# Optimization experiments

Measured on AMD Instinct MI355X. Metric: run time of the kernel, lower is better.

The kernel has to match this reference:

```python
import jax, jax.numpy as jnp
import numpy as np

D_MODEL = 1024
NUM_HEADS = 16
HEAD_DIM = D_MODEL // NUM_HEADS
NEG = -1e9


def setup_inputs() -> dict:
    key = jax.random.key(0)
    kx, kq, kk, kv, ko = jax.random.split(key, 5)
    scale = 1.0 / np.sqrt(D_MODEL)
    x = jax.random.normal(kx, (4, 2048, D_MODEL), dtype=jnp.float32)
    Wq = jax.random.normal(kq, (D_MODEL, D_MODEL), dtype=jnp.float32) * scale
    Wk = jax.random.normal(kk, (D_MODEL, D_MODEL), dtype=jnp.float32) * scale
    Wv = jax.random.normal(kv, (D_MODEL, D_MODEL), dtype=jnp.float32) * scale
    Wo = jax.random.normal(ko, (D_MODEL, D_MODEL), dtype=jnp.float32) * scale
    return {"x": x, "Wq": Wq, "Wk": Wk, "Wv": Wv, "Wo": Wo}


def reference(x, Wq, Wk, Wv, Wo):
    B, S, _ = x.shape
    # torch Linear: y = x @ W.T
    q = (x @ Wq.T).reshape(B, S, NUM_HEADS, HEAD_DIM).transpose(0, 2, 1, 3)
    k = (x @ Wk.T).reshape(B, S, NUM_HEADS, HEAD_DIM).transpose(0, 2, 1, 3)
    v = (x @ Wv.T).reshape(B, S, NUM_HEADS, HEAD_DIM).transpose(0, 2, 1, 3)
    scores = jnp.einsum("bhqd,bhkd->bhqk", q, k) / jnp.sqrt(jnp.float32(HEAD_DIM))
    # additive causal mask: strictly-upper-triangular entries get -1e9 (as in source)
    mask = jnp.triu(jnp.ones((S, S), dtype=scores.dtype), k=1) * NEG
    scores = scores + mask
    attn = jax.nn.softmax(scores, axis=-1)  # dropout p=0.0 -> identity
    out = jnp.einsum("bhqk,bhkd->bhqd", attn, v)
    out = out.transpose(0, 2, 1, 3).reshape(B, S, D_MODEL)
    return out @ Wo.T
```

## Files before the change

### kernel.cpp

```cpp
#include <hip/hip_runtime.h>

typedef __attribute__((ext_vector_type(8))) short short8;
typedef __attribute__((ext_vector_type(4))) short short4v;
typedef __attribute__((ext_vector_type(4))) unsigned short ushort4v;
typedef __attribute__((ext_vector_type(4))) float f32x4;
typedef __attribute__((ext_vector_type(4))) unsigned int u32x4;

static __device__ __forceinline__ unsigned short f2bf(float f){
  unsigned u = __builtin_bit_cast(unsigned, f);
  unsigned r = u + 0x7fffu + ((u >> 16) & 1u);
  return (unsigned short)(r >> 16);
}

static __device__ __forceinline__ float exp2_fast(float x){
  float r; asm("v_exp_f32 %0, %1" : "=v"(r) : "v"(x)); return r;
}

static __device__ __forceinline__ void g2lds16(const unsigned short* g, unsigned short* l){
  __builtin_amdgcn_global_load_lds(
      (const __attribute__((address_space(1))) void*)g,
      (__attribute__((address_space(3))) void*)l, 16, 0, 0);
}

__global__ __launch_bounds__(256) void cast_bf16_kernel(const float* __restrict__ in,
                                                        unsigned short* __restrict__ out, int n8){
  int i = blockIdx.x * 256 + threadIdx.x;
  if (i >= n8) return;
  const float4* p = (const float4*)in + (size_t)i * 2;
  float4 a = p[0], b = p[1];
  short8 o;
  o[0] = (short)f2bf(a.x); o[1] = (short)f2bf(a.y); o[2] = (short)f2bf(a.z); o[3] = (short)f2bf(a.w);
  o[4] = (short)f2bf(b.x); o[5] = (short)f2bf(b.y); o[6] = (short)f2bf(b.z); o[7] = (short)f2bf(b.w);
  *(short8*)(out + (size_t)i * 8) = o;
}

__global__ __launch_bounds__(256) void cast_w4_kernel(const float* __restrict__ w0,
                                                      const float* __restrict__ w1,
                                                      const float* __restrict__ w2,
                                                      const float* __restrict__ w3,
                                                      unsigned short* __restrict__ o0,
                                                      unsigned short* __restrict__ o1,
                                                      unsigned short* __restrict__ o2,
                                                      unsigned short* __restrict__ o3){
  const int z = blockIdx.y;
  const float* in = (z == 0) ? w0 : (z == 1) ? w1 : (z == 2) ? w2 : w3;
  unsigned short* out = (z == 0) ? o0 : (z == 1) ? o1 : (z == 2) ? o2 : o3;
  int i = blockIdx.x * 256 + threadIdx.x;
  const float4* p = (const float4*)in + (size_t)i * 2;
  float4 a = p[0], b = p[1];
  short8 o;
  o[0] = (short)f2bf(a.x); o[1] = (short)f2bf(a.y); o[2] = (short)f2bf(a.z); o[3] = (short)f2bf(a.w);
  o[4] = (short)f2bf(b.x); o[5] = (short)f2bf(b.y); o[6] = (short)f2bf(b.z); o[7] = (short)f2bf(b.w);
  *(short8*)(out + (size_t)i * 8) = o;
}

template<int MODE>
__global__ __launch_bounds__(256) void gemm_nt(
    const unsigned short* __restrict__ A,
    const unsigned short* __restrict__ B0, const unsigned short* __restrict__ B1,
    const unsigned short* __restrict__ B2,
    unsigned short* __restrict__ q0, unsigned short* __restrict__ q1, unsigned short* __restrict__ q2,
    float* __restrict__ fout,
    int M, int N, int K)
{
  __shared__ __attribute__((aligned(16))) unsigned short As[128 * 64];
  __shared__ __attribute__((aligned(16))) unsigned short Bs[128 * 64];
  const int z = blockIdx.y;
  const unsigned short* __restrict__ B = (z == 0) ? B0 : ((z == 1) ? B1 : B2);
  unsigned short* __restrict__ qo = (z == 0) ? q0 : ((z == 1) ? q1 : q2);
  const int ntn = N >> 7;
  const int nwg = gridDim.x, cpx = nwg >> 3;
  const int bid = blockIdx.x;
  const int swz = (bid & 7) * cpx + (bid >> 3);
  const int tm = swz / ntn, tn = swz % ntn;
  const int m0 = tm << 7, n0 = tn << 7;
  const int t = threadIdx.x;
  const int w = t >> 6;
  const int l = t & 63, lo = l & 15, hi = l >> 4;
  const int wr = w >> 1, wc = w & 1;
  f32x4 acc[4][4];
#pragma unroll
  for (int i = 0; i < 4; ++i)
#pragma unroll
    for (int j = 0; j < 4; ++j) acc[i][j] = (f32x4){0.f, 0.f, 0.f, 0.f};

  const int srow = t >> 3;
  const int us = (l & 7) ^ (srow & 7);
  const unsigned short* gA = A + (size_t)(m0 + srow) * K + us * 8;
  const unsigned short* gB = B + (size_t)(n0 + srow) * K + us * 8;

  const int u0 = (((0 * 4 + hi) ^ (lo & 7)) * 8);
  const int u1 = (((1 * 4 + hi) ^ (lo & 7)) * 8);

  for (int kk = 0; kk < K; kk += 64){
#pragma unroll
    for (int i = 0; i < 4; ++i){
      g2lds16(gA + (size_t)(i * 32) * K + kk, &As[i * 2048 + w * 512]);
      g2lds16(gB + (size_t)(i * 32) * K + kk, &Bs[i * 2048 + w * 512]);
    }
    __syncthreads();
#pragma unroll
    for (int kh = 0; kh < 2; ++kh){
      const int uu = kh ? u1 : u0;
      short8 af[4], bf[4];
#pragma unroll
      for (int mf = 0; mf < 4; ++mf)
        af[mf] = *(const short8*)&As[(wr * 64 + mf * 16 + lo) * 64 + uu];
#pragma unroll
      for (int nf = 0; nf < 4; ++nf)
        bf[nf] = *(const short8*)&Bs[(wc * 64 + nf * 16 + lo) * 64 + uu];
      __builtin_amdgcn_s_setprio(1);
#pragma unroll
      for (int mf = 0; mf < 4; ++mf)
#pragma unroll
        for (int nf = 0; nf < 4; ++nf)
          acc[mf][nf] = __builtin_amdgcn_mfma_f32_16x16x32_bf16(af[mf], bf[nf], acc[mf][nf], 0, 0, 0);
      __builtin_amdgcn_s_setprio(0);
    }
    __syncthreads();
  }

#pragma unroll
  for (int mf = 0; mf < 4; ++mf){
#pragma unroll
    for (int nf = 0; nf < 4; ++nf){
      if (MODE == 0 && z == 2){
        int m = m0 + wr * 64 + mf * 16 + hi * 4;
        int n = n0 + wc * 64 + nf * 16 + lo;
        int b = m >> 11, s = m & 2047, h = n >> 6, d = n & 63;
        ushort4v pk4;
        pk4[0] = f2bf(acc[mf][nf][0]);
        pk4[1] = f2bf(acc[mf][nf][1]);
        pk4[2] = f2bf(acc[mf][nf][2]);
        pk4[3] = f2bf(acc[mf][nf][3]);
        *(ushort4v*)&qo[(((size_t)(b * 16 + h)) * 64 + d) * 2048 + s] = pk4;
      } else {
#pragma unroll
        for (int j = 0; j < 4; ++j){
          int m = m0 + wr * 64 + mf * 16 + hi * 4 + j;
          int n = n0 + wc * 64 + nf * 16 + lo;
          float v = acc[mf][nf][j];
          if (MODE == 0){
            int b = m >> 11, s = m & 2047, h = n >> 6, d = n & 63;
            qo[((((size_t)b * 16 + h) * 2048 + s) << 6) + d] = f2bf(v);
          } else {
            fout[(size_t)m * N + n] = v;
          }
        }
      }
    }
  }
}

__global__ __launch_bounds__(256) void attn_kernel(
    const unsigned short* __restrict__ Q, const unsigned short* __restrict__ K,
    const unsigned short* __restrict__ Vt, unsigned short* __restrict__ O)
{
  __shared__ unsigned short Klds[2][64 * 64];
  __shared__ unsigned short Vlds[2][64 * 64];
  const int bid = blockIdx.x;
  const int xcd = bid & 7, rank = bid >> 3;
  const int bh = xcd * 8 + (rank >> 4);
  const int p = rank & 15;
  const int t = threadIdx.x, w = t >> 6, l = t & 63, lo = l & 15, hi = l >> 4;
  const size_t bb = (size_t)bh * 2048 * 64;
  const int bat = bh >> 4, h = bh & 15;
  const int srow0 = w * 8 + (l >> 3);
  const int su0 = l & 7;
  const float cexp = 0.125f * 1.44269504f;

#define STAGE(bufi, kv0) do { \
  _Pragma("unroll") \
  for (int i_ = 0; i_ < 2; ++i_){ \
    int row_ = i_ * 32 + srow0; \
    int us_ = su0 ^ (row_ & 7); \
    g2lds16(&K[bb + (size_t)((kv0) + row_) * 64 + us_ * 8], &Klds[bufi][i_ * 2048 + w * 512]); \
    g2lds16(&Vt[bb + (size_t)row_ * 2048 + (kv0) + us_ * 8], &Vlds[bufi][i_ * 2048 + w * 512]); \
  } \
} while (0)

#pragma unroll 1
  for (int ph = 0; ph < 2; ++ph){
    const int qt = ph ? (31 - p) : p;
    const int qr = qt * 64 + w * 16;
    short8 aq[2];
#pragma unroll
    for (int kg = 0; kg < 2; ++kg)
      aq[kg] = *(const short8*)&Q[bb + (size_t)(qr + lo) * 64 + kg * 32 + hi * 8];
    f32x4 accO[4];
#pragma unroll
    for (int i = 0; i < 4; ++i) accO[i] = (f32x4){0.f, 0.f, 0.f, 0.f};
    float m2 = -3e38f, lsum = 0.f;

    STAGE(0, 0);
    __syncthreads();
    int buf = 0;

#pragma unroll 1
    for (int s = 0; s <= qt; ++s){
      if (s < qt) STAGE(buf ^ 1, (s + 1) * 64);
      const unsigned short* Kl = &Klds[buf][0];
      const unsigned short* Vl = &Vlds[buf][0];
      f32x4 sa[4];
#pragma unroll
      for (int i = 0; i < 4; ++i) sa[i] = (f32x4){0.f, 0.f, 0.f, 0.f};
      __builtin_amdgcn_s_setprio(1);
#pragma unroll
      for (int ni = 0; ni < 4; ++ni)
#pragma unroll
        for (int kg = 0; kg < 2; ++kg){
          int u = (kg * 4 + hi) ^ (lo & 7);
          short8 kf = *(const short8*)&Kl[(ni * 16 + lo) * 64 + u * 8];
          sa[ni] = __builtin_amdgcn_mfma_f32_16x16x32_bf16(kf, aq[kg], sa[ni], 0, 0, 0);
        }
      __builtin_amdgcn_s_setprio(0);
      if (s == qt){
        const int qg = qr + lo;
        const int kv0 = s * 64;
#pragma unroll
        for (int ni = 0; ni < 4; ++ni)
#pragma unroll
          for (int j = 0; j < 4; ++j){
            int kv = kv0 + ni * 16 + hi * 4 + j;
            if (kv > qg) sa[ni][j] = -1e9f;
          }
      }
      float pm = fmaxf(fmaxf(sa[0][0], sa[0][1]), fmaxf(sa[0][2], sa[0][3]));
      pm = fmaxf(pm, fmaxf(fmaxf(sa[1][0], sa[1][1]), fmaxf(sa[1][2], sa[1][3])));
      pm = fmaxf(pm, fmaxf(fmaxf(sa[2][0], sa[2][1]), fmaxf(sa[2][2], sa[2][3])));
      pm = fmaxf(pm, fmaxf(fmaxf(sa[3][0], sa[3][1]), fmaxf(sa[3][2], sa[3][3])));
      float pms = pm * cexp;
      if (!__all(pms <= m2 + 8.0f)){
        float pr = fmaxf(pms, __shfl_xor(pms, 16, 64));
        pr = fmaxf(pr, __shfl_xor(pr, 32, 64));
        float m2n = fmaxf(m2, pr);
        float corr = exp2_fast(m2 - m2n);
        m2 = m2n;
        lsum *= corr;
        float cj[4];
#pragma unroll
        for (int j = 0; j < 4; ++j) cj[j] = __shfl(corr, hi * 4 + j, 64);
#pragma unroll
        for (int dt = 0; dt < 4; ++dt)
#pragma unroll
          for (int j = 0; j < 4; ++j) accO[dt][j] *= cj[j];
      }
      float rs = 0.f;
#pragma unroll
      for (int ni = 0; ni < 4; ++ni)
#pragma unroll
        for (int j = 0; j < 4; ++j){
          float pv = exp2_fast(fmaf(sa[ni][j], cexp, -m2));
          sa[ni][j] = pv;
          rs += pv;
        }
      rs += __shfl_xor(rs, 16, 64);
      rs += __shfl_xor(rs, 32, 64);
      lsum += rs;
      short8 pa[2];
#pragma unroll
      for (int kg = 0; kg < 2; ++kg){
        unsigned r0, r1, r2, r3;
        asm("v_cvt_pk_bf16_f32 %0, %1, %2" : "=v"(r0) : "v"(sa[2*kg][0]),   "v"(sa[2*kg][1]));
        asm("v_cvt_pk_bf16_f32 %0, %1, %2" : "=v"(r1) : "v"(sa[2*kg][2]),   "v"(sa[2*kg][3]));
        asm("v_cvt_pk_bf16_f32 %0, %1, %2" : "=v"(r2) : "v"(sa[2*kg+1][0]), "v"(sa[2*kg+1][1]));
        asm("v_cvt_pk_bf16_f32 %0, %1, %2" : "=v"(r3) : "v"(sa[2*kg+1][2]), "v"(sa[2*kg+1][3]));
        u32x4 pk; pk[0] = r0; pk[1] = r1; pk[2] = r2; pk[3] = r3;
        pa[kg] = __builtin_bit_cast(short8, pk);
      }
      __builtin_amdgcn_s_setprio(1);
#pragma unroll
      for (int dt = 0; dt < 4; ++dt)
#pragma unroll
        for (int kg = 0; kg < 2; ++kg){
          short4v c0, c1;
          {
            int u = ((kg * 2 + 0) * 2 + (hi >> 1)) ^ (lo & 7);
            c0 = *(const short4v*)&Vl[(dt * 16 + lo) * 64 + u * 8 + (hi & 1) * 4];
          }
          {
            int u = ((kg * 2 + 1) * 2 + (hi >> 1)) ^ (lo & 7);
            c1 = *(const short4v*)&Vl[(dt * 16 + lo) * 64 + u * 8 + (hi & 1) * 4];
          }
          short8 vb = (short8){c0[0], c0[1], c0[2], c0[3], c1[0], c1[1], c1[2], c1[3]};
          accO[dt] = __builtin_amdgcn_mfma_f32_16x16x32_bf16(pa[kg], vb, accO[dt], 0, 0, 0);
        }
      __builtin_amdgcn_s_setprio(0);
      __syncthreads();
      buf ^= 1;
    }
    float lr = 1.0f / lsum;
    float lj[4];
#pragma unroll
    for (int j = 0; j < 4; ++j) lj[j] = __shfl(lr, hi * 4 + j, 64);
#pragma unroll
    for (int dt = 0; dt < 4; ++dt)
#pragma unroll
      for (int j = 0; j < 4; ++j){
        int srow = qr + hi * 4 + j;
        O[((size_t)(bat * 2048 + srow) << 10) + h * 64 + dt * 16 + lo] = f2bf(accO[dt][j] * lj[j]);
      }
  }
#undef STAGE
}

extern "C" void kernel_launch(void* const* d_in, const int* in_sizes, int n_in,
                              void* d_out, int out_size, void* d_ws, size_t ws_size,
                              hipStream_t stream){
  (void)in_sizes; (void)n_in; (void)out_size; (void)ws_size;
  const float* x  = (const float*)d_in[0];
  const float* Wq = (const float*)d_in[1];
  const float* Wk = (const float*)d_in[2];
  const float* Wv = (const float*)d_in[3];
  const float* Wo = (const float*)d_in[4];
  char* ws = (char*)d_ws;
  const size_t MB = 1024 * 1024;
  unsigned short* XB  = (unsigned short*)(ws);
  unsigned short* WQB = (unsigned short*)(ws + 16 * MB);
  unsigned short* WKB = (unsigned short*)(ws + 18 * MB);
  unsigned short* WVB = (unsigned short*)(ws + 20 * MB);
  unsigned short* WOB = (unsigned short*)(ws + 22 * MB);
  unsigned short* Qb  = (unsigned short*)(ws + 24 * MB);
  unsigned short* Kb  = (unsigned short*)(ws + 40 * MB);
  unsigned short* Vtb = (unsigned short*)(ws + 56 * MB);
  unsigned short* Ob  = XB;

  cast_bf16_kernel<<<dim3(4096), 256, 0, stream>>>(x, XB, 8388608 / 8);
  cast_w4_kernel<<<dim3(512, 4), 256, 0, stream>>>(Wq, Wk, Wv, Wo, WQB, WKB, WVB, WOB);

  gemm_nt<0><<<dim3(512, 3), 256, 0, stream>>>(XB, WQB, WKB, WVB, Qb, Kb, Vtb, nullptr,
                                               8192, 1024, 1024);
  attn_kernel<<<dim3(1024), 256, 0, stream>>>(Qb, Kb, Vtb, Ob);
  gemm_nt<1><<<dim3(512, 1), 256, 0, stream>>>(Ob, WOB, WOB, WOB, nullptr, nullptr, nullptr,
                                               (float*)d_out, 8192, 1024, 1024);
}
```

Measured before the change: 173.2 us.

## Add 256x128 triple-buffered 8-wave QKV GEMM with interleaved load/MFMA phases

Replaces the QKV projection GEMM with a new kernel that uses 512 threads, a 256x128 output tile and a three-stage LDS ring buffer filled by direct global-to-LDS loads. Each K step is split into four phases that interleave LDS fragment reads, async prefetch of the stage two steps ahead, and MFMA bursts under raised wave priority, in a ping-pong style schedule. The aim is to hide memory latency and raise MFMA utilisation for the largest GEMM. It uses much more LDS per block (about 144 KB), which limits occupancy to one block per CU and adds many barriers.

```diff
diff --git a/kernel.cpp b/kernel.cpp
--- a/kernel.cpp
+++ b/kernel.cpp
@@ -52,6 +52,167 @@
   o[0] = (short)f2bf(a.x); o[1] = (short)f2bf(a.y); o[2] = (short)f2bf(a.z); o[3] = (short)f2bf(a.w);
   o[4] = (short)f2bf(b.x); o[5] = (short)f2bf(b.y); o[6] = (short)f2bf(b.z); o[7] = (short)f2bf(b.w);
   *(short8*)(out + (size_t)i * 8) = o;
+}
+
+__global__ __launch_bounds__(512) void gemm_qkv_8p(
+    const unsigned short* __restrict__ A,
+    const unsigned short* __restrict__ B0, const unsigned short* __restrict__ B1,
+    const unsigned short* __restrict__ B2,
+    unsigned short* __restrict__ q0, unsigned short* __restrict__ q1, unsigned short* __restrict__ q2,
+    int M, int N, int K)
+{
+  __shared__ __attribute__((aligned(16))) unsigned short As[3][256 * 64];
+  __shared__ __attribute__((aligned(16))) unsigned short Bs[3][128 * 64];
+  const int z = blockIdx.y;
+  const unsigned short* __restrict__ B = (z == 0) ? B0 : ((z == 1) ? B1 : B2);
+  unsigned short* __restrict__ qo = (z == 0) ? q0 : ((z == 1) ? q1 : q2);
+  const int ntn = N >> 7;
+  const int nwg = gridDim.x, cpx = nwg >> 3;
+  const int bid = blockIdx.x;
+  const int swz = (bid & 7) * cpx + (bid >> 3);
+  const int tm = swz / ntn, tn = swz % ntn;
+  const int m0 = tm << 8, n0 = tn << 7;
+  const int t = threadIdx.x;
+  const int w = t >> 6, l = t & 63, lo = l & 15, hi = l >> 4;
+  const int wr = w >> 1, wc = w & 1;
+
+  f32x4 acc[4][4];
+#pragma unroll
+  for (int i = 0; i < 4; ++i)
+#pragma unroll
+    for (int j = 0; j < 4; ++j) acc[i][j] = (f32x4){0.f, 0.f, 0.f, 0.f};
+
+  const int srow = t >> 3;
+  const int us = (l & 7) ^ (srow & 7);
+  const unsigned short* gA = A + (size_t)(m0 + srow) * K + us * 8;
+  const unsigned short* gB = B + (size_t)(n0 + srow) * K + us * 8;
+
+  const int u0 = ((0 * 4 + hi) ^ (lo & 7)) * 8;
+  const int u1 = ((1 * 4 + hi) ^ (lo & 7)) * 8;
+
+#define STG_A2(sb, kt2, i0) do { \
+    g2lds16(gA + (size_t)((i0) * 64) * K + (kt2) * 64,        &As[sb][((i0) * 64 + w * 8) * 64]); \
+    g2lds16(gA + (size_t)((i0) * 64 + 64) * K + (kt2) * 64,   &As[sb][((i0) * 64 + 64 + w * 8) * 64]); \
+  } while (0)
+#define STG_B1(sb, kt2, i0) \
+    g2lds16(gB + (size_t)((i0) * 64) * K + (kt2) * 64,        &Bs[sb][((i0) * 64 + w * 8) * 64])
+
+  STG_A2(0, 0, 0); STG_A2(0, 0, 2); STG_B1(0, 0, 0); STG_B1(0, 0, 1);
+  STG_A2(1, 1, 0); STG_A2(1, 1, 2); STG_B1(1, 1, 0); STG_B1(1, 1, 1);
+  asm volatile("s_waitcnt vmcnt(6)" ::: "memory");
+  __builtin_amdgcn_s_barrier();
+  __builtin_amdgcn_sched_barrier(0);
+
+  const int KT = K >> 6;
+  int buf = 0;
+#pragma unroll 1
+  for (int kt = 0; kt < KT; ++kt){
+    const unsigned short* Ab = &As[buf][0];
+    const unsigned short* Bb = &Bs[buf][0];
+    const int sb = (buf >= 1) ? (buf - 1) : 2;
+    const bool st = (kt + 2) < KT;
+    short8 af[4], bf[4];
+
+#pragma unroll
+    for (int mf = 0; mf < 4; ++mf)
+      af[mf] = *(const short8*)&Ab[(wr * 64 + mf * 16 + lo) * 64 + u0];
+    bf[0] = *(const short8*)&Bb[(wc * 64 + 0 * 16 + lo) * 64 + u0];
+    bf[1] = *(const short8*)&Bb[(wc * 64 + 1 * 16 + lo) * 64 + u0];
+    if (st) STG_A2(sb, kt + 2, 0);
+    __builtin_amdgcn_s_barrier();
+    asm volatile("s_waitcnt lgkmcnt(0)" ::: "memory");
+    __builtin_amdgcn_sched_barrier(0);
+    __builtin_amdgcn_s_setprio(1);
+#pragma unroll
+    for (int mf = 0; mf < 4; ++mf){
+      acc[mf][0] = __builtin_amdgcn_mfma_f32_16x16x32_bf16(af[mf], bf[0], acc[mf][0], 0, 0, 0);
+      acc[mf][1] = __builtin_amdgcn_mfma_f32_16x16x32_bf16(af[mf], bf[1], acc[mf][1], 0, 0, 0);
+    }
+    __builtin_amdgcn_s_setprio(0);
+    __builtin_amdgcn_s_barrier();
+
+    bf[2] = *(const short8*)&Bb[(wc * 64 + 2 * 16 + lo) * 64 + u0];
+    bf[3] = *(const short8*)&Bb[(wc * 64 + 3 * 16 + lo) * 64 + u0];
+    if (st) STG_A2(sb, kt + 2, 2);
+    __builtin_amdgcn_s_barrier();
+    asm volatile("s_waitcnt lgkmcnt(0)" ::: "memory");
+    __builtin_amdgcn_sched_barrier(0);
+    __builtin_amdgcn_s_setprio(1);
+#pragma unroll
+    for (int mf = 0; mf < 4; ++mf){
+      acc[mf][2] = __builtin_amdgcn_mfma_f32_16x16x32_bf16(af[mf], bf[2], acc[mf][2], 0, 0, 0);
+      acc[mf][3] = __builtin_amdgcn_mfma_f32_16x16x32_bf16(af[mf], bf[3], acc[mf][3], 0, 0, 0);
+    }
+    __builtin_amdgcn_s_setprio(0);
+    __builtin_amdgcn_s_barrier();
+
+#pragma unroll
+    for (int mf = 0; mf < 4; ++mf)
+      af[mf] = *(const short8*)&Ab[(wr * 64 + mf * 16 + lo) * 64 + u1];
+    bf[0] = *(const short8*)&Bb[(wc * 64 + 0 * 16 + lo) * 64 + u1];
+    bf[1] = *(const short8*)&Bb[(wc * 64 + 1 * 16 + lo) * 64 + u1];
+    if (st) STG_B1(sb, kt + 2, 0);
+    __builtin_amdgcn_s_barrier();
+    asm volatile("s_waitcnt lgkmcnt(0)" ::: "memory");
+    __builtin_amdgcn_sched_barrier(0);
+    __builtin_amdgcn_s_setprio(1);
+#pragma unroll
+    for (int mf = 0; mf < 4; ++mf){
+      acc[mf][0] = __builtin_amdgcn_mfma_f32_16x16x32_bf16(af[mf], bf[0], acc[mf][0], 0, 0, 0);
+      acc[mf][1] = __builtin_amdgcn_mfma_f32_16x16x32_bf16(af[mf], bf[1], acc[mf][1], 0, 0, 0);
+    }
+    __builtin_amdgcn_s_setprio(0);
+    __builtin_amdgcn_s_barrier();
+
+    bf[2] = *(const short8*)&Bb[(wc * 64 + 2 * 16 + lo) * 64 + u1];
+    bf[3] = *(const short8*)&Bb[(wc * 64 + 3 * 16 + lo) * 64 + u1];
+    if (st) STG_B1(sb, kt + 2, 1);
+    __builtin_amdgcn_s_barrier();
+    asm volatile("s_waitcnt lgkmcnt(0)" ::: "memory");
+    __builtin_amdgcn_sched_barrier(0);
+    __builtin_amdgcn_s_setprio(1);
+#pragma unroll
+    for (int mf = 0; mf < 4; ++mf){
+      acc[mf][2] = __builtin_amdgcn_mfma_f32_16x16x32_bf16(af[mf], bf[2], acc[mf][2], 0, 0, 0);
+      acc[mf][3] = __builtin_amdgcn_mfma_f32_16x16x32_bf16(af[mf], bf[3], acc[mf][3], 0, 0, 0);
+    }
+    __builtin_amdgcn_s_setprio(0);
+    if (kt + 1 < KT){
+      if (kt + 2 < KT) asm volatile("s_waitcnt vmcnt(6)" ::: "memory");
+      else             asm volatile("s_waitcnt vmcnt(0)" ::: "memory");
+    }
+    __builtin_amdgcn_s_barrier();
+    __builtin_amdgcn_sched_barrier(0);
+    buf = (buf == 2) ? 0 : buf + 1;
+  }
+#undef STG_A2
+#undef STG_B1
+
+#pragma unroll
+  for (int mf = 0; mf < 4; ++mf){
+#pragma unroll
+    for (int nf = 0; nf < 4; ++nf){
+      if (z == 2){
+        int m = m0 + wr * 64 + mf * 16 + hi * 4;
+        int n = n0 + wc * 64 + nf * 16 + lo;
+        int b = m >> 11, s = m & 2047, h = n >> 6, d = n & 63;
+        ushort4v pk4;
+        pk4[0] = f2bf(acc[mf][nf][0]);
+        pk4[1] = f2bf(acc[mf][nf][1]);
+        pk4[2] = f2bf(acc[mf][nf][2]);
+        pk4[3] = f2bf(acc[mf][nf][3]);
+        *(ushort4v*)&qo[(((size_t)(b * 16 + h)) * 64 + d) * 2048 + s] = pk4;
+      } else {
+#pragma unroll
+        for (int j = 0; j < 4; ++j){
+          int m = m0 + wr * 64 + mf * 16 + hi * 4 + j;
+          int n = n0 + wc * 64 + nf * 16 + lo;
+          int b = m >> 11, s = m & 2047, h = n >> 6, d = n & 63;
+          qo[((((size_t)b * 16 + h) * 2048 + s) << 6) + d] = f2bf(acc[mf][nf][j]);
+        }
+      }
+    }
+  }
 }
 
 template<int MODE>
@@ -328,8 +489,8 @@
   cast_bf16_kernel<<<dim3(4096), 256, 0, stream>>>(x, XB, 8388608 / 8);
   cast_w4_kernel<<<dim3(512, 4), 256, 0, stream>>>(Wq, Wk, Wv, Wo, WQB, WKB, WVB, WOB);
 
-  gemm_nt<0><<<dim3(512, 3), 256, 0, stream>>>(XB, WQB, WKB, WVB, Qb, Kb, Vtb, nullptr,
-                                               8192, 1024, 1024);
+  gemm_qkv_8p<<<dim3(256, 3), 512, 0, stream>>>(XB, WQB, WKB, WVB, Qb, Kb, Vtb,
+                                                8192, 1024, 1024);
   attn_kernel<<<dim3(1024), 256, 0, stream>>>(Qb, Kb, Vtb, Ob);
   gemm_nt<1><<<dim3(512, 1), 256, 0, stream>>>(Ob, WOB, WOB, WOB, nullptr, nullptr, nullptr,
                                                (float*)d_out, 8192, 1024, 1024);
```

New measurement: 190.2 us. 1.1x slower.
